# Optimization experiments

Measured on AMD Instinct MI355X. Metric: run time of the kernel, lower is better.

## Reference

```python
import jax, jax.numpy as jnp
import numpy as np

NUM_VIEWS = 6
NUM_HEADS = 16
NUM_LAYERS = 2
DIST_THRESHOLD = 10.0
EPS = 1e-5


def layer_norm(x, g, b):
    m = jnp.mean(x, axis=-1, keepdims=True)
    v = jnp.mean((x - m) ** 2, axis=-1, keepdims=True)
    return (x - m) / jnp.sqrt(v + EPS) * g + b


def build_mask(coords3d, num_views, threshold):
    # coords3d: (B, T, 3) -> bool mask (B, T, T), True = masked
    B, T, _ = coords3d.shape
    tpv = T // num_views
    c = jnp.nan_to_num(coords3d, nan=0.0, posinf=100.0, neginf=-100.0)
    view_ids = jnp.repeat(jnp.arange(num_views), tpv)
    same_view = view_ids[:, None] == view_ids[None, :]  # (T, T)
    dist_sq = jnp.sum((c[:, :, None, :] - c[:, None, :, :]) ** 2, axis=-1)  # (B,T,T)
    mask = same_view[None] | (dist_sq > threshold * threshold)
    all_masked = jnp.all(mask, axis=-1)  # (B, T)
    eye = jnp.eye(T, dtype=bool)
    # unmask diagonal for rows that are fully masked (matches torch fix)
    mask = jnp.where(all_masked[:, :, None] & eye[None], False, mask)
    return mask


def mha(x, qkv_w, qkv_b, out_w, out_b, mask, num_heads):
    # x: (B,T,C); qkv_w: (3C,C); out_w: (C,C); mask: (B,T,T) True=masked
    B, T, C = x.shape
    hd = C // num_heads
    qkv = x @ qkv_w.T + qkv_b  # (B,T,3C)
    q, k, v = jnp.split(qkv, 3, axis=-1)
    def heads(t):
        return t.reshape(B, T, num_heads, hd).transpose(0, 2, 1, 3)  # (B,H,T,hd)
    q, k, v = heads(q), heads(k), heads(v)
    scale = 1.0 / jnp.sqrt(jnp.asarray(hd, x.dtype))
    scores = jnp.einsum('bhqd,bhkd->bhqk', q * scale, k)
    scores = jnp.where(mask[:, None], -jnp.inf, scores)
    attn = jax.nn.softmax(scores, axis=-1)
    o = jnp.einsum('bhqk,bhkd->bhqd', attn, v)  # (B,H,T,hd)
    o = o.transpose(0, 2, 1, 3).reshape(B, T, C)
    return o @ out_w.T + out_b


def setup_inputs() -> dict:
    key = jax.random.key(0)
    B, T, C, L = 2, 1536, 1024, NUM_LAYERS
    ks = jax.random.split(key, 16)
    s = 0.02
    inp = {
        'pos_embed': jax.random.normal(ks[0], (B, T, C), jnp.float32),
        'coords3d': jax.random.normal(ks[1], (B, T, 3), jnp.float32) * 8.0,
        'ln1_g': jnp.ones((L, C), jnp.float32),
        'ln1_b': jnp.zeros((L, C), jnp.float32),
        'qkv_w': jax.random.normal(ks[2], (L, 3 * C, C), jnp.float32) * s,
        'qkv_b': jnp.zeros((L, 3 * C), jnp.float32),
        'out_w': jax.random.normal(ks[3], (L, C, C), jnp.float32) * s,
        'out_b': jnp.zeros((L, C), jnp.float32),
        'ln2_g': jnp.ones((L, C), jnp.float32),
        'ln2_b': jnp.zeros((L, C), jnp.float32),
        'ffn_w1': jax.random.normal(ks[4], (L, 4 * C, C), jnp.float32) * s,
        'ffn_b1': jnp.zeros((L, 4 * C), jnp.float32),
        'ffn_w2': jax.random.normal(ks[5], (L, C, 4 * C), jnp.float32) * s,
        'ffn_b2': jnp.zeros((L, C), jnp.float32),
        'norm_g': jnp.ones((C,), jnp.float32),
        'norm_b': jnp.zeros((C,), jnp.float32),
    }
    return inp


def reference(pos_embed, coords3d, ln1_g, ln1_b, qkv_w, qkv_b, out_w, out_b,
              ln2_g, ln2_b, ffn_w1, ffn_b1, ffn_w2, ffn_b2, norm_g, norm_b):
    mask = build_mask(coords3d, NUM_VIEWS, DIST_THRESHOLD)
    x = pos_embed
    for l in range(NUM_LAYERS):
        xn = layer_norm(x, ln1_g[l], ln1_b[l])
        x = x + mha(xn, qkv_w[l], qkv_b[l], out_w[l], out_b[l], mask, NUM_HEADS)
        xn = layer_norm(x, ln2_g[l], ln2_b[l])
        h = jax.nn.gelu(xn @ ffn_w1[l].T + ffn_b1[l], approximate=False)
        x = x + (h @ ffn_w2[l].T + ffn_b2[l])
    return layer_norm(x, norm_g, norm_b)
```

## Files before the change

kernel.cpp:

```cpp
#include <hip/hip_runtime.h>

#define TT 1536
#define CC 1024
#define NH 16
#define HD 64
#define NL 2
#define NB 2
#define MM (NB*TT)

typedef unsigned short u16;
typedef unsigned int u32;
typedef unsigned long long u64;
typedef __attribute__((ext_vector_type(8))) short short8v;
typedef __attribute__((ext_vector_type(4))) float f32x4;

__device__ __forceinline__ u16 f2bf(float f){
  u32 u = __float_as_uint(f);
  u32 r = (u + 0x7FFFu + ((u >> 16) & 1u)) >> 16;
  return (u16)r;
}

__device__ __forceinline__ u16 f2bfc(float f){
  return (u16)((__float_as_uint(f) + 0x8000u) >> 16);
}

__device__ __forceinline__ void gload_lds16(const void* g, void* l){
  __builtin_amdgcn_global_load_lds(
      (const __attribute__((address_space(1))) void*)g,
      (__attribute__((address_space(3))) void*)l, 16, 0, 0);
}

__device__ __forceinline__ f32x4 mfma16(short8v a, short8v b, f32x4 c){
  return __builtin_amdgcn_mfma_f32_16x16x32_bf16(a, b, c, 0, 0, 0);
}

__device__ __forceinline__ char* ldsw(void* base, int row, int colb){
  return (char*)base + row * 128 + (colb ^ ((row & 7) << 4));
}

__device__ __forceinline__ short bf16_eighth(short x){
  float f = __uint_as_float(((u32)(u16)x) << 16) * 0.125f;
  return (short)(u16)(__float_as_uint(f) >> 16);
}

__global__ __launch_bounds__(256) void cvt_bf16_kernel(const float* __restrict__ in,
                                                       u16* __restrict__ out, int n4){
  int stride = gridDim.x * 256;
  for (int i = blockIdx.x * 256 + threadIdx.x; i < n4; i += stride){
    const float4 v = ((const float4*)in)[i];
    ushort4 o;
    o.x = f2bf(v.x); o.y = f2bf(v.y); o.z = f2bf(v.z); o.w = f2bf(v.w);
    ((ushort4*)out)[i] = o;
  }
}

__device__ __forceinline__ float fixc(float v){
  if (__builtin_isnan(v)) return 0.0f;
  if (__builtin_isinf(v)) return v > 0.0f ? 100.0f : -100.0f;
  return v;
}

__global__ __launch_bounds__(256) void mask_kernel(const float* __restrict__ coords,
                                                   u64* __restrict__ maskw){
  const int tid = threadIdx.x, wave = tid >> 6, lane = tid & 63;
  const int ri = blockIdx.x * 4 + wave;
  const int b = ri / TT, i = ri - b * TT;
  const float* cp = coords + (size_t)ri * 3;
  const float cx = fixc(cp[0]), cy = fixc(cp[1]), cz = fixc(cp[2]);
  const int vi = i >> 8;
  u64 allm = ~0ull;
  for (int ch = 0; ch < 24; ++ch){
    const int j = ch * 64 + lane;
    const float* cj = coords + ((size_t)b * TT + j) * 3;
    const float dx = cx - fixc(cj[0]);
    const float dy = cy - fixc(cj[1]);
    const float dz = cz - fixc(cj[2]);
    const float d2 = dx*dx + dy*dy + dz*dz;
    const bool masked = ((j >> 8) == vi) || (d2 > 100.0f);
    const u64 bal = __ballot(masked);
    if (lane == 0) maskw[(size_t)ri * 24 + ch] = bal;
    allm &= bal;
  }
  if (lane == 0 && allm == ~0ull){
    const size_t w = (size_t)ri * 24 + (i >> 6);
    maskw[w] &= ~(1ull << (i & 63));
  }
}

template<int OUTF>
__global__ __launch_bounds__(256) void ln_kernel(const float* __restrict__ x,
    const float* __restrict__ gw, const float* __restrict__ bw,
    u16* __restrict__ outb, float* __restrict__ outf){
  __shared__ float sred[4];
  const int tid = threadIdx.x, wave = tid >> 6, lane = tid & 63;
  const size_t row = blockIdx.x;
  const float4 v = *(const float4*)(x + row * CC + tid * 4);
  float s = v.x + v.y + v.z + v.w;
  #pragma unroll
  for (int o = 1; o < 64; o <<= 1) s += __shfl_xor(s, o, 64);
  if (lane == 0) sred[wave] = s;
  __syncthreads();
  const float mean = (sred[0] + sred[1] + sred[2] + sred[3]) * (1.0f / CC);
  __syncthreads();
  const float d0 = v.x - mean, d1 = v.y - mean, d2 = v.z - mean, d3 = v.w - mean;
  float q = d0*d0 + d1*d1 + d2*d2 + d3*d3;
  #pragma unroll
  for (int o = 1; o < 64; o <<= 1) q += __shfl_xor(q, o, 64);
  if (lane == 0) sred[wave] = q;
  __syncthreads();
  const float var = (sred[0] + sred[1] + sred[2] + sred[3]) * (1.0f / CC);
  const float rstd = rsqrtf(var + 1e-5f);
  const float4 g4 = *(const float4*)(gw + tid * 4);
  const float4 b4 = *(const float4*)(bw + tid * 4);
  const float y0 = d0 * rstd * g4.x + b4.x;
  const float y1 = d1 * rstd * g4.y + b4.y;
  const float y2 = d2 * rstd * g4.z + b4.z;
  const float y3 = d3 * rstd * g4.w + b4.w;
  if (OUTF){
    *(float4*)(outf + row * CC + tid * 4) = make_float4(y0, y1, y2, y3);
  } else {
    ushort4 o4; o4.x = f2bf(y0); o4.y = f2bf(y1); o4.z = f2bf(y2); o4.w = f2bf(y3);
    *(ushort4*)(outb + row * CC + tid * 4) = o4;
  }
}

template<int EPI>
__global__ __launch_bounds__(512, 4) void gemm_nt(const u16* __restrict__ A,
    const u16* __restrict__ Bw, const float* __restrict__ bias,
    const float* __restrict__ res, u16* __restrict__ outb, float* __restrict__ outf,
    int M, int N, int K){
  __shared__ u16 As[2][128][64];
  __shared__ u16 Bs[2][128][64];
  const int tid = threadIdx.x, wave = tid >> 6, lane = tid & 63;
  const int gx = gridDim.x;
  const int nwg = gx * gridDim.y;
  const int orig = blockIdx.y * gx + blockIdx.x;
  const int qq = nwg >> 3, rm = nwg & 7;
  const int xcd = orig & 7, pos = orig >> 3;
  const int wg = (xcd < rm ? xcd * (qq + 1) : rm * (qq + 1) + (xcd - rm) * qq) + pos;
  const int m0 = (wg / gx) * 128, n0 = (wg % gx) * 128;
  const int wr = wave >> 1, wc = wave & 1;
  f32x4 acc[2][4];
  #pragma unroll
  for (int mi = 0; mi < 2; ++mi)
    #pragma unroll
    for (int ni = 0; ni < 4; ++ni){ f32x4 z = {0.f,0.f,0.f,0.f}; acc[mi][ni] = z; }

  const u16* Ag = A + (size_t)m0 * K;
  const u16* Bg = Bw + (size_t)n0 * K;
  const int srow0 = wave * 8 + (lane >> 3);
  const int scole = ((lane & 7) ^ (lane >> 3)) * 8;
  auto stage = [&](int buf, int k0){
    char* ab = (char*)&As[buf][0][0];
    char* bb = (char*)&Bs[buf][0][0];
    #pragma unroll
    for (int l = 0; l < 2; ++l){
      const size_t goff = (size_t)(l*64 + srow0) * K + k0 + scole;
      const int loff = (l*8 + wave) * 1024;
      gload_lds16(Ag + goff, ab + loff);
      gload_lds16(Bg + goff, bb + loff);
    }
  };

  const int NT = K >> 6;
  stage(0, 0);
  stage(1, 64);

  const int ar = lane & 15, akb = (lane >> 4) * 16;
  const int rsw = (ar & 7) << 4;
  for (int t = 0; t < NT; ++t){
    const int cur = t & 1;
    if (t + 1 < NT) asm volatile("s_waitcnt vmcnt(4)" ::: "memory");
    else            asm volatile("s_waitcnt vmcnt(0)" ::: "memory");
    __builtin_amdgcn_s_barrier();
    const char* ab = (const char*)&As[cur][0][0];
    const char* bb = (const char*)&Bs[cur][0][0];
    short8v af[2][2], bf[4][2];
    #pragma unroll
    for (int ks = 0; ks < 2; ++ks){
      const int cb = (ks*64 + akb) ^ rsw;
      #pragma unroll
      for (int mi = 0; mi < 2; ++mi)
        af[mi][ks] = *(const short8v*)(ab + (wr*32 + mi*16 + ar)*128 + cb);
      #pragma unroll
      for (int ni = 0; ni < 4; ++ni)
        bf[ni][ks] = *(const short8v*)(bb + (wc*64 + ni*16 + ar)*128 + cb);
    }
    asm volatile("s_waitcnt lgkmcnt(0)" ::: "memory");
    __builtin_amdgcn_sched_barrier(0);
    __builtin_amdgcn_s_barrier();
    if (t + 2 < NT) stage(cur, (t + 2) * 64);
    __builtin_amdgcn_s_setprio(1);
    #pragma unroll
    for (int ks = 0; ks < 2; ++ks)
      #pragma unroll
      for (int mi = 0; mi < 2; ++mi)
        #pragma unroll
        for (int ni = 0; ni < 4; ++ni)
          acc[mi][ni] = mfma16(af[mi][ks], bf[ni][ks], acc[mi][ni]);
    __builtin_amdgcn_s_setprio(0);
  }

  const int cr = (lane >> 4) * 4, cl = lane & 15;
  #pragma unroll
  for (int ni = 0; ni < 4; ++ni){
    const int c = n0 + wc*64 + ni*16 + cl;
    const float bv = bias[c];
    #pragma unroll
    for (int mi = 0; mi < 2; ++mi){
      #pragma unroll
      for (int r = 0; r < 4; ++r){
        const size_t rr2 = (size_t)(m0 + wr*32 + mi*16 + cr + r);
        float v = acc[mi][ni][r] + bv;
        if constexpr (EPI == 1) v = 0.5f * v * (1.0f + erff(v * 0.70710678118654752f));
        if constexpr (EPI == 2) outf[rr2 * N + c] = v + res[rr2 * N + c];
        else outb[rr2 * N + c] = f2bf(v);
      }
    }
  }
}

__global__ __launch_bounds__(256) void attn_kernel(const u16* __restrict__ qkv,
    const u64* __restrict__ maskw, u16* __restrict__ outp){
  __shared__ u16 Ks[2][64][64];
  __shared__ u16 Vt[2][64][64];
  __shared__ u16 Ps[4][16][64];
  const int tid = threadIdx.x, wave = tid >> 6, lane = tid & 63;
  const int b = blockIdx.y >> 4, h = blockIdx.y & 15;
  const int qb = blockIdx.x * 64;
  const int rs = 3 * CC;
  const int g4 = lane >> 4;
  const int l15 = lane & 15;
  const int qrow = qb + wave * 16 + l15;

  const u16* qp = qkv + (size_t)(b * TT + qrow) * rs + h * HD + g4 * 8;
  short8v qf0, qf1;
  {
    const short8v r0 = *(const short8v*)qp;
    const short8v r1 = *(const short8v*)(qp + 32);
    #pragma unroll
    for (int e = 0; e < 8; ++e){ qf0[e] = bf16_eighth(r0[e]); qf1[e] = bf16_eighth(r1[e]); }
  }

  f32x4 o[4];
  #pragma unroll
  for (int dt = 0; dt < 4; ++dt){ f32x4 z = {0.f,0.f,0.f,0.f}; o[dt] = z; }
  float m_r = -1e30f, l_r = 0.f;

  u16* psb = &Ps[wave][0][0];
  const u64* mrow_p = maskw + (size_t)(b * TT + qrow) * 24;

  auto stageK = [&](int t, int buf){
    const int j0 = t * 64;
    #pragma unroll
    for (int l = 0; l < 2; ++l){
      const int off = (wave * 2 + l) * 1024;
      const int krow = (off >> 7) + (lane >> 3);
      const int kcolb = ((lane & 7) * 16) ^ ((krow & 7) << 4);
      gload_lds16(qkv + (size_t)(b * TT + j0 + krow) * rs + CC + h * HD + (kcolb >> 1),
                  (char*)(&Ks[buf][0][0]) + off);
    }
  };
  u16 vv[16];
  auto loadV = [&](int t){
    const int j0 = t * 64;
    #pragma unroll
    for (int it = 0; it < 2; ++it){
      const int jc = it * 4 + wave;
      #pragma unroll
      for (int e = 0; e < 8; ++e)
        vv[it*8+e] = qkv[(size_t)(b * TT + j0 + jc * 8 + e) * rs + 2 * CC + h * HD + lane];
    }
  };
  auto writeV = [&](int buf){
    #pragma unroll
    for (int it = 0; it < 2; ++it){
      const int jc = it * 4 + wave;
      short8v sv;
      #pragma unroll
      for (int e = 0; e < 8; ++e) sv[e] = (short)vv[it*8+e];
      *(short8v*)ldsw(&Vt[buf][0][0], lane, jc * 16) = sv;
    }
  };

  loadV(0);
  stageK(0, 0);
  writeV(0);
  __syncthreads();

  for (int t = 0; t < TT / 64; ++t){
    const int cur = t & 1;
    const bool pf = (t < TT / 64 - 1);
    if (pf){ loadV(t + 1); stageK(t + 1, cur ^ 1); }

    const u64 mw = mrow_p[t];

    const char* Kc = (const char*)&Ks[cur][0][0];
    f32x4 S[4];
    #pragma unroll
    for (int jt = 0; jt < 4; ++jt){
      const short8v k0 = *(const short8v*)ldsw((void*)Kc, jt*16 + l15, g4 * 16);
      const short8v k1 = *(const short8v*)ldsw((void*)Kc, jt*16 + l15, 64 + g4 * 16);
      f32x4 z = {0.f,0.f,0.f,0.f};
      z = mfma16(k0, qf0, z);
      z = mfma16(k1, qf1, z);
      S[jt] = z;
    }

    float ps[16]; u32 pmask = 0;
    float cmax = -1e30f;
    #pragma unroll
    for (int jt = 0; jt < 4; ++jt){
      const u32 mj = (u32)(mw >> (jt * 16 + g4 * 4)) & 0xFu;
      #pragma unroll
      for (int r = 0; r < 4; ++r){
        float s = S[jt][r];
        s = ((mj >> r) & 1u) ? -1e30f : s;
        ps[jt*4+r] = s;
        cmax = fmaxf(cmax, s);
      }
      pmask |= mj << (jt * 4);
    }
    cmax = fmaxf(cmax, __shfl_xor(cmax, 16));
    cmax = fmaxf(cmax, __shfl_xor(cmax, 32));
    const float mnew = fmaxf(m_r, cmax);
    const float fac = __expf(m_r - mnew);
    m_r = mnew;
    float psum = 0.f;
    #pragma unroll
    for (int i = 0; i < 16; ++i){
      const float p = ((pmask >> i) & 1u) ? 0.f : __expf(ps[i] - mnew);
      ps[i] = p; psum += p;
    }
    psum += __shfl_xor(psum, 16);
    psum += __shfl_xor(psum, 32);
    l_r = l_r * fac + psum;

    float fr4[4];
    #pragma unroll
    for (int r = 0; r < 4; ++r) fr4[r] = __shfl(fac, g4 * 4 + r);
    #pragma unroll
    for (int dt = 0; dt < 4; ++dt){
      f32x4 tt = o[dt];
      tt[0] *= fr4[0]; tt[1] *= fr4[1]; tt[2] *= fr4[2]; tt[3] *= fr4[3];
      o[dt] = tt;
    }

    #pragma unroll
    for (int jt = 0; jt < 4; ++jt){
      ushort4 pk;
      pk.x = f2bfc(ps[jt*4+0]); pk.y = f2bfc(ps[jt*4+1]);
      pk.z = f2bfc(ps[jt*4+2]); pk.w = f2bfc(ps[jt*4+3]);
      *(ushort4*)ldsw(psb, l15, jt * 32 + g4 * 8) = pk;
    }

    short8v pA[2];
    #pragma unroll
    for (int kc = 0; kc < 2; ++kc)
      pA[kc] = *(const short8v*)ldsw(psb, l15, kc * 64 + g4 * 16);
    char* Vc = (char*)&Vt[cur][0][0];
    #pragma unroll
    for (int dt = 0; dt < 4; ++dt){
      #pragma unroll
      for (int kc = 0; kc < 2; ++kc){
        const short8v vf = *(const short8v*)ldsw(Vc, dt*16 + l15, kc * 64 + g4 * 16);
        o[dt] = mfma16(pA[kc], vf, o[dt]);
      }
    }

    if (pf) writeV(cur ^ 1);
    __syncthreads();
  }

  const float linv = (l_r > 0.f) ? 1.0f / l_r : 0.f;
  float lr4[4];
  #pragma unroll
  for (int r = 0; r < 4; ++r) lr4[r] = __shfl(linv, g4 * 4 + r);
  #pragma unroll
  for (int dt = 0; dt < 4; ++dt)
    #pragma unroll
    for (int r = 0; r < 4; ++r)
      outp[(size_t)(b * TT + qb + wave * 16 + g4 * 4 + r) * CC + h * HD + dt * 16 + l15] =
          f2bf(o[dt][r] * lr4[r]);
}

extern "C" void kernel_launch(void* const* d_in, const int* in_sizes, int n_in,
                              void* d_out, int out_size, void* d_ws, size_t ws_size,
                              hipStream_t stream){
  (void)in_sizes; (void)n_in; (void)out_size; (void)ws_size;
  const float* pos    = (const float*)d_in[0];
  const float* coords = (const float*)d_in[1];
  const float* ln1g   = (const float*)d_in[2];
  const float* ln1b   = (const float*)d_in[3];
  const float* qkvw   = (const float*)d_in[4];
  const float* qkvbi  = (const float*)d_in[5];
  const float* outw   = (const float*)d_in[6];
  const float* outbi  = (const float*)d_in[7];
  const float* ln2g   = (const float*)d_in[8];
  const float* ln2b   = (const float*)d_in[9];
  const float* w1     = (const float*)d_in[10];
  const float* b1     = (const float*)d_in[11];
  const float* w2     = (const float*)d_in[12];
  const float* b2     = (const float*)d_in[13];
  const float* ng     = (const float*)d_in[14];
  const float* nbb    = (const float*)d_in[15];

  char* wsp = (char*)d_ws;
  size_t off = 0;
  auto alloc = [&](size_t bytes)->void*{
    void* p = wsp + off; off += (bytes + 255) & ~(size_t)255; return p;
  };
  u16* qkvw_bf = (u16*)alloc((size_t)NL*3*CC*CC*sizeof(u16));
  u16* outw_bf = (u16*)alloc((size_t)NL*CC*CC*sizeof(u16));
  u16* w1_bf   = (u16*)alloc((size_t)NL*4*CC*CC*sizeof(u16));
  u16* w2_bf   = (u16*)alloc((size_t)NL*4*CC*CC*sizeof(u16));
  float* x     = (float*)alloc((size_t)MM*CC*sizeof(float));
  u16* xn      = (u16*)alloc((size_t)MM*CC*sizeof(u16));
  u16* qkvbuf  = (u16*)alloc((size_t)MM*4*CC*sizeof(u16));
  u16* attnb   = (u16*)alloc((size_t)MM*CC*sizeof(u16));
  u64* maskw   = (u64*)alloc((size_t)MM*24*sizeof(u64));
  u16* hbuf = qkvbuf;

  auto cvt = [&](const float* s, u16* dst, size_t n){
    int n4 = (int)(n >> 2);
    int blocks = (n4 + 255) / 256; if (blocks > 4096) blocks = 4096;
    cvt_bf16_kernel<<<dim3(blocks), dim3(256), 0, stream>>>(s, dst, n4);
  };
  cvt(qkvw, qkvw_bf, (size_t)NL*3*CC*CC);
  cvt(outw, outw_bf, (size_t)NL*CC*CC);
  cvt(w1, w1_bf, (size_t)NL*4*CC*CC);
  cvt(w2, w2_bf, (size_t)NL*4*CC*CC);

  hipMemcpyAsync(x, pos, (size_t)MM*CC*sizeof(float), hipMemcpyDeviceToDevice, stream);
  mask_kernel<<<dim3(MM/4), dim3(256), 0, stream>>>(coords, maskw);

  for (int l = 0; l < NL; ++l){
    ln_kernel<0><<<dim3(MM), dim3(256), 0, stream>>>(x, ln1g + l*CC, ln1b + l*CC, xn, nullptr);
    gemm_nt<0><<<dim3(3*CC/128, MM/128), dim3(512), 0, stream>>>(
        xn, qkvw_bf + (size_t)l*3*CC*CC, qkvbi + l*3*CC, nullptr, qkvbuf, nullptr, MM, 3*CC, CC);
    attn_kernel<<<dim3(TT/64, NB*NH), dim3(256), 0, stream>>>(qkvbuf, maskw, attnb);
    gemm_nt<2><<<dim3(CC/128, MM/128), dim3(512), 0, stream>>>(
        attnb, outw_bf + (size_t)l*CC*CC, outbi + l*CC, x, nullptr, x, MM, CC, CC);
    ln_kernel<0><<<dim3(MM), dim3(256), 0, stream>>>(x, ln2g + l*CC, ln2b + l*CC, xn, nullptr);
    gemm_nt<1><<<dim3(4*CC/128, MM/128), dim3(512), 0, stream>>>(
        xn, w1_bf + (size_t)l*4*CC*CC, b1 + l*4*CC, nullptr, hbuf, nullptr, MM, 4*CC, CC);
    gemm_nt<2><<<dim3(CC/128, MM/128), dim3(512), 0, stream>>>(
        hbuf, w2_bf + (size_t)l*4*CC*CC, b2 + l*CC, x, nullptr, x, MM, CC, 4*CC);
  }
  ln_kernel<1><<<dim3(MM), dim3(256), 0, stream>>>(x, ng, nbb, nullptr, (float*)d_out);
}
```

Measured before the change: 477.6 us.

## Streamline attention softmax: exp2 with folded log2e, lazy rescale, MFMA row sums

Folds log2(e)/sqrt(hd) into the Q scaling so the softmax can use the hardware exp2. The running max is only updated and the output rescaled when a new block max exceeds it by more than a threshold (wave-uniform check). Row sums are computed by an extra MFMA against a ones vector instead of shuffles and scalar adds, and bf16 packing uses v_cvt_pk_bf16_f32. The goal is to cut VALU and shuffle work in the softmax inner loop, at the cost of two extra MFMAs per tile and a looser numerical bound from the lazy max.

```diff
diff --git a/kernel.cpp b/kernel.cpp
--- a/kernel.cpp
+++ b/kernel.cpp
@@ -20,10 +20,6 @@
   return (u16)r;
 }
 
-__device__ __forceinline__ u16 f2bfc(float f){
-  return (u16)((__float_as_uint(f) + 0x8000u) >> 16);
-}
-
 __device__ __forceinline__ void gload_lds16(const void* g, void* l){
   __builtin_amdgcn_global_load_lds(
       (const __attribute__((address_space(1))) void*)g,
@@ -34,13 +30,18 @@
   return __builtin_amdgcn_mfma_f32_16x16x32_bf16(a, b, c, 0, 0, 0);
 }
 
+__device__ __forceinline__ float exp2f_fast(float x){
+  return __builtin_amdgcn_exp2f(x);
+}
+
+__device__ __forceinline__ u32 cvt_pk_bf16(float lo, float hi){
+  u32 r;
+  asm("v_cvt_pk_bf16_f32 %0, %1, %2" : "=v"(r) : "v"(lo), "v"(hi));
+  return r;
+}
+
 __device__ __forceinline__ char* ldsw(void* base, int row, int colb){
   return (char*)base + row * 128 + (colb ^ ((row & 7) << 4));
-}
-
-__device__ __forceinline__ short bf16_eighth(short x){
-  float f = __uint_as_float(((u32)(u16)x) << 16) * 0.125f;
-  return (short)(u16)(__float_as_uint(f) >> 16);
 }
 
 __global__ __launch_bounds__(256) void cvt_bf16_kernel(const float* __restrict__ in,
@@ -233,22 +234,31 @@
   const int l15 = lane & 15;
   const int qrow = qb + wave * 16 + l15;
 
+  const float qscale = 0.18033688011112042f;
   const u16* qp = qkv + (size_t)(b * TT + qrow) * rs + h * HD + g4 * 8;
   short8v qf0, qf1;
   {
     const short8v r0 = *(const short8v*)qp;
     const short8v r1 = *(const short8v*)(qp + 32);
     #pragma unroll
-    for (int e = 0; e < 8; ++e){ qf0[e] = bf16_eighth(r0[e]); qf1[e] = bf16_eighth(r1[e]); }
-  }
-
-  f32x4 o[4];
+    for (int e = 0; e < 8; ++e){
+      qf0[e] = (short)f2bf(__uint_as_float(((u32)(u16)r0[e]) << 16) * qscale);
+      qf1[e] = (short)f2bf(__uint_as_float(((u32)(u16)r1[e]) << 16) * qscale);
+    }
+  }
+
+  f32x4 o[4], lacc;
   #pragma unroll
   for (int dt = 0; dt < 4; ++dt){ f32x4 z = {0.f,0.f,0.f,0.f}; o[dt] = z; }
-  float m_r = -1e30f, l_r = 0.f;
+  { f32x4 z = {0.f,0.f,0.f,0.f}; lacc = z; }
+  float m_r = -1.0e4f;
 
   u16* psb = &Ps[wave][0][0];
   const u64* mrow_p = maskw + (size_t)(b * TT + qrow) * 24;
+
+  short8v vone;
+  #pragma unroll
+  for (int e = 0; e < 8; ++e) vone[e] = (short)0x3F80;
 
   auto stageK = [&](int t, int buf){
     const int j0 = t * 64;
@@ -294,6 +304,7 @@
     if (pf){ loadV(t + 1); stageK(t + 1, cur ^ 1); }
 
     const u64 mw = mrow_p[t];
+    const u32 mwlo = (u32)mw, mwhi = (u32)(mw >> 32);
 
     const char* Kc = (const char*)&Ks[cur][0][0];
     f32x4 S[4];
@@ -307,51 +318,48 @@
       S[jt] = z;
     }
 
-    float ps[16]; u32 pmask = 0;
-    float cmax = -1e30f;
+    float ps[16];
+    float cmax = -3.0e38f;
     #pragma unroll
     for (int jt = 0; jt < 4; ++jt){
-      const u32 mj = (u32)(mw >> (jt * 16 + g4 * 4)) & 0xFu;
+      const u32 msrc = (jt & 2) ? mwhi : mwlo;
+      const int sh = g4 * 4 + (jt & 1) * 16;
       #pragma unroll
       for (int r = 0; r < 4; ++r){
         float s = S[jt][r];
-        s = ((mj >> r) & 1u) ? -1e30f : s;
+        s = ((msrc >> (sh + r)) & 1u) ? -3.0e38f : s;
         ps[jt*4+r] = s;
         cmax = fmaxf(cmax, s);
       }
-      pmask |= mj << (jt * 4);
     }
     cmax = fmaxf(cmax, __shfl_xor(cmax, 16));
     cmax = fmaxf(cmax, __shfl_xor(cmax, 32));
-    const float mnew = fmaxf(m_r, cmax);
-    const float fac = __expf(m_r - mnew);
-    m_r = mnew;
-    float psum = 0.f;
-    #pragma unroll
-    for (int i = 0; i < 16; ++i){
-      const float p = ((pmask >> i) & 1u) ? 0.f : __expf(ps[i] - mnew);
-      ps[i] = p; psum += p;
-    }
-    psum += __shfl_xor(psum, 16);
-    psum += __shfl_xor(psum, 32);
-    l_r = l_r * fac + psum;
-
-    float fr4[4];
-    #pragma unroll
-    for (int r = 0; r < 4; ++r) fr4[r] = __shfl(fac, g4 * 4 + r);
-    #pragma unroll
-    for (int dt = 0; dt < 4; ++dt){
-      f32x4 tt = o[dt];
-      tt[0] *= fr4[0]; tt[1] *= fr4[1]; tt[2] *= fr4[2]; tt[3] *= fr4[3];
-      o[dt] = tt;
-    }
+
+    if (!__all(cmax <= m_r + 8.0f)){
+      const float mnew = fmaxf(m_r, cmax);
+      const float fac = exp2f_fast(m_r - mnew);
+      m_r = mnew;
+      float fr4[4];
+      #pragma unroll
+      for (int r = 0; r < 4; ++r) fr4[r] = __shfl(fac, g4 * 4 + r);
+      #pragma unroll
+      for (int dt = 0; dt < 4; ++dt){
+        f32x4 tt = o[dt];
+        tt[0] *= fr4[0]; tt[1] *= fr4[1]; tt[2] *= fr4[2]; tt[3] *= fr4[3];
+        o[dt] = tt;
+      }
+      lacc[0] *= fr4[0]; lacc[1] *= fr4[1]; lacc[2] *= fr4[2]; lacc[3] *= fr4[3];
+    }
+
+    #pragma unroll
+    for (int i = 0; i < 16; ++i) ps[i] = exp2f_fast(ps[i] - m_r);
 
     #pragma unroll
     for (int jt = 0; jt < 4; ++jt){
-      ushort4 pk;
-      pk.x = f2bfc(ps[jt*4+0]); pk.y = f2bfc(ps[jt*4+1]);
-      pk.z = f2bfc(ps[jt*4+2]); pk.w = f2bfc(ps[jt*4+3]);
-      *(ushort4*)ldsw(psb, l15, jt * 32 + g4 * 8) = pk;
+      uint2 pk;
+      pk.x = cvt_pk_bf16(ps[jt*4+0], ps[jt*4+1]);
+      pk.y = cvt_pk_bf16(ps[jt*4+2], ps[jt*4+3]);
+      *(uint2*)ldsw(psb, l15, jt * 32 + g4 * 8) = pk;
     }
 
     short8v pA[2];
@@ -367,21 +375,22 @@
         o[dt] = mfma16(pA[kc], vf, o[dt]);
       }
     }
+    lacc = mfma16(pA[0], vone, lacc);
+    lacc = mfma16(pA[1], vone, lacc);
 
     if (pf) writeV(cur ^ 1);
     __syncthreads();
   }
 
-  const float linv = (l_r > 0.f) ? 1.0f / l_r : 0.f;
-  float lr4[4];
-  #pragma unroll
-  for (int r = 0; r < 4; ++r) lr4[r] = __shfl(linv, g4 * 4 + r);
+  float linv[4];
+  #pragma unroll
+  for (int r = 0; r < 4; ++r) linv[r] = 1.0f / fmaxf(lacc[r], 1e-30f);
   #pragma unroll
   for (int dt = 0; dt < 4; ++dt)
     #pragma unroll
     for (int r = 0; r < 4; ++r)
       outp[(size_t)(b * TT + qb + wave * 16 + g4 * 4 + r) * CC + h * HD + dt * 16 + l15] =
-          f2bf(o[dt][r] * lr4[r]);
+          f2bf(o[dt][r] * linv[r]);
 }
 
 extern "C" void kernel_launch(void* const* d_in, const int* in_sizes, int n_in,
```

Result: faster. 461.4 us (-3.4%).
